# Kernel optimization log

Hardware: AMD Instinct MI355X
Metric: run time of the kernel (lower is better)

The kernel has to match this reference:

```python
import jax, jax.numpy as jnp
import numpy as np

B, T, DIM, H = 4, 2048, 1024, 16
HD = DIM // H  # 64
ROPE_BASE = 10000.0


def _rope_cos_sin(seq_len, head_dim, dtype):
    # lucidrains rotary-embedding-torch convention: interleaved pairs.
    inv_freq = 1.0 / (ROPE_BASE ** (jnp.arange(0, head_dim, 2, dtype=jnp.float32) / head_dim))
    freqs = jnp.arange(seq_len, dtype=jnp.float32)[:, None] * inv_freq[None, :]  # [T, hd/2]
    freqs = jnp.repeat(freqs, 2, axis=-1)  # [T, hd], each freq duplicated for the pair
    return jnp.cos(freqs).astype(dtype), jnp.sin(freqs).astype(dtype)


def _rotate_half(x):
    # interleaved pairs: (x1, x2) -> (-x2, x1)
    x = x.reshape(*x.shape[:-1], -1, 2)
    x1, x2 = x[..., 0], x[..., 1]
    return jnp.stack([-x2, x1], axis=-1).reshape(*x.shape[:-2], -1)


def _apply_rope(x, cos, sin):
    # x: [B, H, T, hd]; cos/sin: [T, hd]
    return x * cos[None, None, :, :] + _rotate_half(x) * sin[None, None, :, :]


def setup_inputs() -> dict:
    key = jax.random.key(0)
    kx, kqkv, kw, kb = jax.random.split(key, 4)
    s_qkv = 1.0 / np.sqrt(DIM)
    return {
        "x": jax.random.normal(kx, (B, T, DIM), dtype=jnp.float32),
        "w_qkv": jax.random.normal(kqkv, (3 * DIM, DIM), dtype=jnp.float32) * s_qkv,
        "w_proj": jax.random.normal(kw, (DIM, DIM), dtype=jnp.float32) * s_qkv,
        "b_proj": jax.random.normal(kb, (DIM,), dtype=jnp.float32) * 0.01,
    }


def reference(x, w_qkv, w_proj, b_proj):
    b, t, c = x.shape
    qkv = jnp.einsum('btc,dc->btd', x, w_qkv)  # [B, T, 3*C]
    qkv = qkv.reshape(b, t, 3, H, HD).transpose(2, 0, 3, 1, 4)  # [3, B, H, T, hd]
    q, k, v = qkv[0], qkv[1], qkv[2]

    cos, sin = _rope_cos_sin(t, HD, x.dtype)
    q = _apply_rope(q, cos, sin)
    k = _apply_rope(k, cos, sin)

    scale = 1.0 / np.sqrt(HD)
    scores = jnp.einsum('bhqd,bhkd->bhqk', q, k) * scale  # [B, H, T, T]
    attn = jax.nn.softmax(scores, axis=-1)
    out = jnp.einsum('bhqk,bhkd->bhqd', attn, v)  # [B, H, T, hd]

    out = out.transpose(0, 2, 1, 3).reshape(b, t, c)  # [B, T, C]
    return jnp.einsum('btc,dc->btd', out, w_proj) + b_proj
```

## Files before the change

kernel.cpp:

```cpp
#include <hip/hip_runtime.h>
#include <hip/hip_bf16.h>
#include <math.h>

#define Bz   4
#define Tz   2048
#define DIMz 1024
#define Hz   16
#define HDz  64
#define BHz  (Bz*Hz)
#define Mz   (Bz*Tz)
#define LOG2E 1.44269504088896340736f
#define QSCALE (0.125f * LOG2E)

typedef __attribute__((ext_vector_type(8)))  __bf16 bf16x8;
typedef __attribute__((ext_vector_type(4)))  __bf16 bf16x4;
typedef __attribute__((ext_vector_type(2)))  __bf16 bf16x2;
typedef __attribute__((ext_vector_type(4)))  float  f32x4;
typedef __attribute__((ext_vector_type(16))) float  f32x16;

__device__ __forceinline__ f32x4 mfma_16x16x32(bf16x8 a, bf16x8 b, f32x4 c) {
  return __builtin_amdgcn_mfma_f32_16x16x32_bf16(a, b, c, 0, 0, 0);
}
__device__ __forceinline__ f32x16 mfma_32x32x16(bf16x8 a, bf16x8 b, f32x16 c) {
  return __builtin_amdgcn_mfma_f32_32x32x16_bf16(a, b, c, 0, 0, 0);
}

__device__ __forceinline__ ushort f2bf(float f) {
  unsigned u = __float_as_uint(f);
  u += 0x7fffu + ((u >> 16) & 1u);
  return (ushort)(u >> 16);
}

__device__ __forceinline__ float fast_exp2(float x) {
#if __has_builtin(__builtin_amdgcn_exp2f)
  return __builtin_amdgcn_exp2f(x);
#else
  float r;
  asm("v_exp_f32 %0, %1\n\ts_nop 1" : "=v"(r) : "v"(x));
  return r;
#endif
}

__device__ __forceinline__ void gl_lds16(const ushort* g, ushort* l) {
  __builtin_amdgcn_global_load_lds(
      (const __attribute__((address_space(1))) unsigned int*)g,
      (__attribute__((address_space(3))) unsigned int*)l, 16, 0, 0);
}

#define N4_X   (Mz * DIMz / 4)
#define N4_WQ  (3 * DIMz * DIMz / 4)
#define N4_WP  (DIMz * DIMz / 4)
__global__ void k_cvt3(const float4* __restrict__ x,  ushort4* __restrict__ ox,
                       const float4* __restrict__ wq, ushort4* __restrict__ owq,
                       const float4* __restrict__ wp, ushort4* __restrict__ owp) {
  int i = blockIdx.x * blockDim.x + threadIdx.x;
  const float4* in; ushort4* out;
  if (i < N4_X)                { in = x + i;                 out = ox + i; }
  else if (i < N4_X + N4_WQ)   { in = wq + (i - N4_X);       out = owq + (i - N4_X); }
  else if (i < N4_X + N4_WQ + N4_WP) { in = wp + (i - N4_X - N4_WQ); out = owp + (i - N4_X - N4_WQ); }
  else return;
  float4 v = *in;
  ushort4 o;
  o.x = f2bf(v.x); o.y = f2bf(v.y); o.z = f2bf(v.z); o.w = f2bf(v.w);
  *out = o;
}

__global__ void k_rope_tab(float* __restrict__ tab) {
  int idx = blockIdx.x * blockDim.x + threadIdx.x;
  if (idx >= Tz * 32) return;
  int t = idx >> 5, i = idx & 31;
  double ang = (double)t * exp(((double)(-2 * i) / (double)HDz) * log(10000.0));
  tab[2 * idx]     = (float)cos(ang);
  tab[2 * idx + 1] = (float)sin(ang);
}


__global__ __launch_bounds__(256) void k_gemm_qkv(const ushort* __restrict__ A,
                                                  const ushort* __restrict__ Bw,
                                                  const float* __restrict__ tab,
                                                  ushort* __restrict__ qb,
                                                  ushort* __restrict__ kb,
                                                  ushort* __restrict__ vbt) {
  __shared__ ushort As[128 * 64];
  __shared__ ushort Bs[128 * 64];
  const int tid = threadIdx.x;
  const int xcd = blockIdx.x & 7;
  const int ib  = blockIdx.x >> 3;
  const int bm  = (xcd * 8 + (ib & 7)) << 7;
  const int bn  = (ib >> 3) << 7;
  const int wid = tid >> 6, lane = tid & 63;
  const int wr = (wid & 1) << 6, wc = (wid >> 1) << 6;
  const int lr = lane & 15, lg = lane >> 4;

  const int r8 = lane >> 3;
  const int cswz = (((lane & 7) ^ r8) << 3);
  const ushort* pA = A  + (size_t)(bm + wid * 8 + r8) * 1024 + cswz;
  const ushort* pB = Bw + (size_t)(bn + wid * 8 + r8) * 1024 + cswz;
  ushort* lA = &As[wid * 512];
  ushort* lB = &Bs[wid * 512];

  const int cs0 = ((lg ^ (lr & 7)) << 3);
  const int cs1 = cs0 ^ 32;

  const f32x4 fz = {0.f, 0.f, 0.f, 0.f};
  f32x4 acc[4][4];
  #pragma unroll
  for (int i = 0; i < 4; i++)
    #pragma unroll
    for (int j = 0; j < 4; j++) acc[i][j] = fz;

  for (int k0 = 0; k0 < 1024; k0 += 64) {
    __syncthreads();
    #pragma unroll
    for (int rep = 0; rep < 4; rep++) {
      gl_lds16(pA + (size_t)rep * 32768 + k0, lA + rep * 2048);
      gl_lds16(pB + (size_t)rep * 32768 + k0, lB + rep * 2048);
    }
    __syncthreads();
    #pragma unroll
    for (int kc = 0; kc < 2; kc++) {
      const int cs = kc ? cs1 : cs0;
      bf16x8 af[4], bfr[4];
      #pragma unroll
      for (int i = 0; i < 4; i++)
        af[i] = *reinterpret_cast<const bf16x8*>(&As[(wr + i * 16 + lr) * 64 + cs]);
      #pragma unroll
      for (int j = 0; j < 4; j++)
        bfr[j] = *reinterpret_cast<const bf16x8*>(&Bs[(wc + j * 16 + lr) * 64 + cs]);
      #pragma unroll
      for (int i = 0; i < 4; i++)
        #pragma unroll
        for (int j = 0; j < 4; j++)
          acc[i][j] = mfma_16x16x32(af[i], bfr[j], acc[i][j]);
    }
  }

  #pragma unroll
  for (int j = 0; j < 4; j++) {
    int col = bn + wc + j * 16 + lr;
    int which = col >> 10;
    int r = col & 1023;
    int h = r >> 6, hd = r & 63;
    #pragma unroll
    for (int i = 0; i < 4; i++) {
      int row0 = bm + wr + i * 16 + lg * 4;
      int b = row0 >> 11, t0 = row0 & 2047;
      if (which == 2) {
        int t0p = (t0 & ~12) | ((t0 & 4) << 1) | ((t0 & 8) >> 1);
        uint lo = (uint)f2bf(acc[i][j][0]) | ((uint)f2bf(acc[i][j][1]) << 16);
        uint hi = (uint)f2bf(acc[i][j][2]) | ((uint)f2bf(acc[i][j][3]) << 16);
        *reinterpret_cast<uint2*>(&vbt[((size_t)(b * Hz + h) * HDz + hd) * Tz + t0p]) =
            make_uint2(lo, hi);
      } else {
        ushort* dst = (which == 0) ? qb : kb;
        const float sc = (which == 0) ? QSCALE : 1.0f;
        const float sgn = (hd & 1) ? 1.0f : -1.0f;
        const float* tb = &tab[((size_t)t0 * 32 + (hd >> 1)) * 2];
        #pragma unroll
        for (int q = 0; q < 4; q++) {
          float own = acc[i][j][q];
          float other = __shfl_xor(own, 1);
          float c = tb[q * 64], s = tb[q * 64 + 1];
          dst[(((size_t)(b * Hz + h) * Tz + t0 + q) << 6) + hd] =
              f2bf((own * c + sgn * other * s) * sc);
        }
      }
    }
  }
}

__global__ __launch_bounds__(256, 4) void k_attn(const ushort* __restrict__ qb,
                                                 const ushort* __restrict__ kbp,
                                                 const ushort* __restrict__ vbt,
                                                 ushort* __restrict__ ao) {
  __shared__ ushort Ks0[64 * 64], Ks1[64 * 64], Ks2[64 * 64];
  __shared__ ushort Vs0[64 * 64], Vs1[64 * 64];

  const int bid = ((blockIdx.x & 7) << 7) + (blockIdx.x >> 3);
  const int qt = bid & 15;
  const int bh = bid >> 4;
  const int tid = threadIdx.x, wid = tid >> 6, lane = tid & 63;
  const int l31 = lane & 31, hi = lane >> 5;

  const ushort* Kg = kbp + (size_t)bh * Tz * HDz;
  const ushort* Vg = vbt + (size_t)bh * HDz * Tz;

  const ushort* Qrow = qb + ((size_t)bh * Tz + qt * 128 + wid * 32 + l31) * HDz + hi * 8;
  bf16x8 qf[4];
  #pragma unroll
  for (int m = 0; m < 4; m++)
    qf[m] = *reinterpret_cast<const bf16x8*>(Qrow + m * 16);

  const int r8 = lane >> 3;
  const int c0 = (((lane & 7) ^ r8 ^ ((2 * wid) & 3)) << 3);
  const int c1 = (((lane & 7) ^ r8 ^ ((2 * wid + 1) & 3)) << 3);
  const ushort* kp0 = Kg + (size_t)(wid * 16 + r8) * 64 + c0;
  const ushort* kp1 = Kg + (size_t)(wid * 16 + 8 + r8) * 64 + c1;
  const ushort* vp0 = Vg + (size_t)(wid * 16 + r8) * Tz + c0;
  const ushort* vp1 = Vg + (size_t)(wid * 16 + 8 + r8) * Tz + c1;

  f32x16 oacc0, oacc1;
  #pragma unroll
  for (int i = 0; i < 16; i++) { oacc0[i] = 0.f; oacc1[i] = 0.f; }
  float lrun = 0.f;

  const int swr = (lane & 7) ^ ((lane >> 3) & 3);
  int csk[4];
  #pragma unroll
  for (int m = 0; m < 4; m++) csk[m] = ((2 * m + hi) ^ swr) << 3;

  union FP { uint u[4]; bf16x8 v; };

  ushort *kb_cur = Ks0, *kb_nxt = Ks1, *kb_pre = Ks2;
  ushort *vb_cur = Vs0, *vb_nxt = Vs1;

  gl_lds16(kp0, kb_cur + wid * 1024); gl_lds16(kp1, kb_cur + wid * 1024 + 512);
  gl_lds16(kp0 + 4096, kb_nxt + wid * 1024); gl_lds16(kp1 + 4096, kb_nxt + wid * 1024 + 512);
  gl_lds16(vp0, vb_cur + wid * 1024); gl_lds16(vp1, vb_cur + wid * 1024 + 512);
  asm volatile("s_waitcnt vmcnt(4)" ::: "memory");
  __builtin_amdgcn_s_barrier();

  const int NT = Tz / 64;
  for (int kt = 0; kt < NT; kt++) {
    if (kt + 2 < NT) {
      gl_lds16(kp0 + (size_t)(kt + 2) * 4096, kb_pre + wid * 1024);
      gl_lds16(kp1 + (size_t)(kt + 2) * 4096, kb_pre + wid * 1024 + 512);
    }

    f32x16 sA, sB;
    #pragma unroll
    for (int i = 0; i < 16; i++) { sA[i] = 0.f; sB[i] = 0.f; }
    __builtin_amdgcn_s_setprio(1);
    #pragma unroll
    for (int m = 0; m < 4; m++) {
      bf16x8 kfA = *reinterpret_cast<const bf16x8*>(&kb_cur[l31 * 64 + csk[m]]);
      bf16x8 kfB = *reinterpret_cast<const bf16x8*>(&kb_cur[(32 + l31) * 64 + csk[m]]);
      sA = mfma_32x32x16(kfA, qf[m], sA);
      sB = mfma_32x32x16(kfB, qf[m], sB);
    }
    __builtin_amdgcn_s_setprio(0);

    float rs = 0.f;
    FP fA0, fA1, fB0, fB1;
    #pragma unroll
    for (int i = 0; i < 4; i++) {
      float e00 = fast_exp2(sA[2 * i]);
      float e01 = fast_exp2(sA[2 * i + 1]);
      float e10 = fast_exp2(sA[8 + 2 * i]);
      float e11 = fast_exp2(sA[9 + 2 * i]);
      rs += (e00 + e01) + (e10 + e11);
      bf16x2 t0, t1;
      t0[0] = (__bf16)e00; t0[1] = (__bf16)e01;
      t1[0] = (__bf16)e10; t1[1] = (__bf16)e11;
      fA0.u[i] = *reinterpret_cast<uint*>(&t0);
      fA1.u[i] = *reinterpret_cast<uint*>(&t1);
    }
    #pragma unroll
    for (int i = 0; i < 4; i++) {
      float e00 = fast_exp2(sB[2 * i]);
      float e01 = fast_exp2(sB[2 * i + 1]);
      float e10 = fast_exp2(sB[8 + 2 * i]);
      float e11 = fast_exp2(sB[9 + 2 * i]);
      rs += (e00 + e01) + (e10 + e11);
      bf16x2 t0, t1;
      t0[0] = (__bf16)e00; t0[1] = (__bf16)e01;
      t1[0] = (__bf16)e10; t1[1] = (__bf16)e11;
      fB0.u[i] = *reinterpret_cast<uint*>(&t0);
      fB1.u[i] = *reinterpret_cast<uint*>(&t1);
    }
    rs += __shfl_xor(rs, 32);
    lrun += rs;

    asm volatile("s_waitcnt vmcnt(2)" ::: "memory");
    __builtin_amdgcn_s_barrier();

    if (kt + 1 < NT) {
      gl_lds16(vp0 + (kt + 1) * 64, vb_nxt + wid * 1024);
      gl_lds16(vp1 + (kt + 1) * 64, vb_nxt + wid * 1024 + 512);
    }

    __builtin_amdgcn_s_setprio(1);
    #pragma unroll
    for (int blk = 0; blk < 2; blk++) {
      const ushort* vrow = &vb_cur[(blk * 32 + l31) * 64];
      bf16x8 vf0 = *reinterpret_cast<const bf16x8*>(vrow + csk[0]);
      bf16x8 vf1 = *reinterpret_cast<const bf16x8*>(vrow + csk[1]);
      bf16x8 vf2 = *reinterpret_cast<const bf16x8*>(vrow + csk[2]);
      bf16x8 vf3 = *reinterpret_cast<const bf16x8*>(vrow + csk[3]);
      f32x16 o = blk ? oacc1 : oacc0;
      o = mfma_32x32x16(fA0.v, vf0, o);
      o = mfma_32x32x16(fA1.v, vf1, o);
      o = mfma_32x32x16(fB0.v, vf2, o);
      o = mfma_32x32x16(fB1.v, vf3, o);
      if (blk) oacc1 = o; else oacc0 = o;
    }
    __builtin_amdgcn_s_setprio(0);

    ushort* t0 = kb_cur; kb_cur = kb_nxt; kb_nxt = kb_pre; kb_pre = t0;
    ushort* t1 = vb_cur; vb_cur = vb_nxt; vb_nxt = t1;
  }

  const int b = bh >> 4, h = bh & 15;
  #pragma unroll
  for (int r = 0; r < 16; r++) {
    int qrow = (r & 3) + 8 * (r >> 2) + 4 * hi;
    float inv = 1.0f / __shfl(lrun, qrow);
    int t = qt * 128 + wid * 32 + qrow;
    size_t base = ((size_t)(b * Tz + t) * Hz + h) * HDz;
    ao[base + l31]      = f2bf(oacc0[r] * inv);
    ao[base + 32 + l31] = f2bf(oacc1[r] * inv);
  }
}

__global__ __launch_bounds__(256) void k_gemm_proj(const ushort* __restrict__ A,
                                                   const ushort* __restrict__ Bw,
                                                   const float* __restrict__ bias,
                                                   float* __restrict__ out) {
  __shared__ ushort As[128 * 64];
  __shared__ ushort Bs[128 * 64];
  const int tid = threadIdx.x;
  const int xcd = blockIdx.x & 7;
  const int ib  = blockIdx.x >> 3;
  const int bm  = (xcd * 8 + (ib & 7)) << 7;
  const int bn  = (ib >> 3) << 7;
  const int wid = tid >> 6, lane = tid & 63;
  const int wr = (wid & 1) << 6, wc = (wid >> 1) << 6;
  const int lr = lane & 15, lg = lane >> 4;

  const int r8 = lane >> 3;
  const int cswz = (((lane & 7) ^ r8) << 3);
  const ushort* pA = A  + (size_t)(bm + wid * 8 + r8) * 1024 + cswz;
  const ushort* pB = Bw + (size_t)(bn + wid * 8 + r8) * 1024 + cswz;
  ushort* lA = &As[wid * 512];
  ushort* lB = &Bs[wid * 512];

  const int cs0 = ((lg ^ (lr & 7)) << 3);
  const int cs1 = cs0 ^ 32;

  const f32x4 fz = {0.f, 0.f, 0.f, 0.f};
  f32x4 acc[4][4];
  #pragma unroll
  for (int i = 0; i < 4; i++)
    #pragma unroll
    for (int j = 0; j < 4; j++) acc[i][j] = fz;

  for (int k0 = 0; k0 < 1024; k0 += 64) {
    __syncthreads();
    #pragma unroll
    for (int rep = 0; rep < 4; rep++) {
      gl_lds16(pA + (size_t)rep * 32768 + k0, lA + rep * 2048);
      gl_lds16(pB + (size_t)rep * 32768 + k0, lB + rep * 2048);
    }
    __syncthreads();
    #pragma unroll
    for (int kc = 0; kc < 2; kc++) {
      const int cs = kc ? cs1 : cs0;
      bf16x8 af[4], bfr[4];
      #pragma unroll
      for (int i = 0; i < 4; i++)
        af[i] = *reinterpret_cast<const bf16x8*>(&As[(wr + i * 16 + lr) * 64 + cs]);
      #pragma unroll
      for (int j = 0; j < 4; j++)
        bfr[j] = *reinterpret_cast<const bf16x8*>(&Bs[(wc + j * 16 + lr) * 64 + cs]);
      #pragma unroll
      for (int i = 0; i < 4; i++)
        #pragma unroll
        for (int j = 0; j < 4; j++)
          acc[i][j] = mfma_16x16x32(af[i], bfr[j], acc[i][j]);
    }
  }

  #pragma unroll
  for (int j = 0; j < 4; j++) {
    int col = bn + wc + j * 16 + lr;
    float bv = bias[col];
    #pragma unroll
    for (int i = 0; i < 4; i++) {
      #pragma unroll
      for (int q = 0; q < 4; q++) {
        int row = bm + wr + i * 16 + lg * 4 + q;
        out[(size_t)row * 1024 + col] = acc[i][j][q] + bv;
      }
    }
  }
}

extern "C" void kernel_launch(void* const* d_in, const int* in_sizes, int n_in,
                              void* d_out, int out_size, void* d_ws, size_t ws_size,
                              hipStream_t stream) {
  const float* x      = (const float*)d_in[0];
  const float* w_qkv  = (const float*)d_in[1];
  const float* w_proj = (const float*)d_in[2];
  const float* b_proj = (const float*)d_in[3];
  float* out = (float*)d_out;

  char* ws = (char*)d_ws;
  ushort* xh     = (ushort*)ws; ws += (size_t)Mz * DIMz * 2;
  ushort* wqkvh  = (ushort*)ws; ws += (size_t)3 * DIMz * DIMz * 2;
  ushort* wprojh = (ushort*)ws; ws += (size_t)DIMz * DIMz * 2;
  ushort* qbuf   = (ushort*)ws; ws += (size_t)BHz * Tz * HDz * 2;
  ushort* kbuf   = (ushort*)ws; ws += (size_t)BHz * Tz * HDz * 2;
  ushort* vbuft  = (ushort*)ws; ws += (size_t)BHz * HDz * Tz * 2;
  ushort* aout   = (ushort*)ws; ws += (size_t)Mz * DIMz * 2;
  float*  tab    = (float*)ws;  ws += (size_t)Tz * 32 * 2 * 4;

  k_cvt3<<<(N4_X + N4_WQ + N4_WP + 255) / 256, 256, 0, stream>>>(
      (const float4*)x, (ushort4*)xh,
      (const float4*)w_qkv, (ushort4*)wqkvh,
      (const float4*)w_proj, (ushort4*)wprojh);
  k_rope_tab<<<256, 256, 0, stream>>>(tab);
  k_gemm_qkv<<<64 * 24, 256, 0, stream>>>(xh, wqkvh, tab, qbuf, kbuf, vbuft);
  k_attn<<<BHz * (Tz / 128), 256, 0, stream>>>(qbuf, kbuf, vbuft, aout);
  k_gemm_proj<<<64 * 8, 256, 0, stream>>>(aout, wprojh, b_proj, out);
}
```

Before: 186.9 us.

## Triple-buffer GEMM LDS tiles with async prefetch and MFMA priority

Replaces the synchronous load-then-compute K loop in both the QKV and projection GEMMs with a three-stage LDS ring of 32-wide K tiles. Global-to-LDS loads for tile k+2 are issued before computing tile k, and partial vmcnt waits plus raw barriers replace the full syncthreads pairs. The MFMA block is wrapped in s_setprio to favour matrix issue. The aim is to hide global load latency behind compute, at the cost of more barriers (one per 32-wide K step), a new swizzle scheme, and hand-counted waitcnt values that must match the number of outstanding loads.

```diff
diff --git a/kernel.cpp b/kernel.cpp
--- a/kernel.cpp
+++ b/kernel.cpp
@@ -75,14 +75,73 @@
 }
 
 
+#define GEMM_PRE(Aptr, Bptr, bmv, bnv)                                              \
+  const int q4 = lane >> 2;                                                         \
+  const int cSW = (((lane & 3) ^ ((lane >> 3) & 3)) << 3);                          \
+  const ushort* sA = (Aptr) + (size_t)((bmv) + wid * 32 + q4) * 1024 + cSW;         \
+  const ushort* sB = (Bptr) + (size_t)((bnv) + wid * 32 + q4) * 1024 + cSW;         \
+  const int csf = ((lg ^ ((lr >> 1) & 3)) << 3);                                    \
+  ushort *aCur = SA0, *aNxt = SA1, *aPre = SA2;                                     \
+  ushort *bCur = SB0, *bNxt = SB1, *bPre = SB2;
+
+#define GEMM_STAGE(t, aDst, bDst)                                                   \
+  do {                                                                              \
+    gl_lds16(sA + (t) * 32, (aDst) + wid * 1024);                                   \
+    gl_lds16(sA + (t) * 32 + 16 * 1024, (aDst) + wid * 1024 + 512);                 \
+    gl_lds16(sB + (t) * 32, (bDst) + wid * 1024);                                   \
+    gl_lds16(sB + (t) * 32 + 16 * 1024, (bDst) + wid * 1024 + 512);                 \
+  } while (0)
+
+#define GEMM_COMPUTE()                                                              \
+  do {                                                                              \
+    bf16x8 af[4], bfr[4];                                                           \
+    _Pragma("unroll")                                                               \
+    for (int i = 0; i < 4; i++)                                                     \
+      af[i] = *reinterpret_cast<const bf16x8*>(&aCur[(wr + i * 16 + lr) * 32 + csf]); \
+    _Pragma("unroll")                                                               \
+    for (int j = 0; j < 4; j++)                                                     \
+      bfr[j] = *reinterpret_cast<const bf16x8*>(&bCur[(wc + j * 16 + lr) * 32 + csf]); \
+    __builtin_amdgcn_s_setprio(1);                                                  \
+    _Pragma("unroll")                                                               \
+    for (int i = 0; i < 4; i++)                                                     \
+      _Pragma("unroll")                                                             \
+      for (int j = 0; j < 4; j++)                                                   \
+        acc[i][j] = mfma_16x16x32(af[i], bfr[j], acc[i][j]);                        \
+    __builtin_amdgcn_s_setprio(0);                                                  \
+  } while (0)
+
+#define GEMM_ROTATE()                                                               \
+  do {                                                                              \
+    ushort* t0_ = aCur; aCur = aNxt; aNxt = aPre; aPre = t0_;                       \
+    ushort* t1_ = bCur; bCur = bNxt; bNxt = bPre; bPre = t1_;                       \
+  } while (0)
+
+#define GEMM_MAIN()                                                                 \
+  GEMM_STAGE(0, aCur, bCur);                                                        \
+  GEMM_STAGE(1, aNxt, bNxt);                                                        \
+  asm volatile("s_waitcnt vmcnt(4)" ::: "memory");                                  \
+  __builtin_amdgcn_s_barrier();                                                     \
+  for (int kt = 0; kt < 30; kt++) {                                                 \
+    GEMM_STAGE(kt + 2, aPre, bPre);                                                 \
+    GEMM_COMPUTE();                                                                 \
+    asm volatile("s_waitcnt vmcnt(4)" ::: "memory");                                \
+    __builtin_amdgcn_s_barrier();                                                   \
+    GEMM_ROTATE();                                                                  \
+  }                                                                                 \
+  GEMM_COMPUTE();                                                                   \
+  asm volatile("s_waitcnt vmcnt(0)" ::: "memory");                                  \
+  __builtin_amdgcn_s_barrier();                                                     \
+  GEMM_ROTATE();                                                                    \
+  GEMM_COMPUTE();
+
 __global__ __launch_bounds__(256) void k_gemm_qkv(const ushort* __restrict__ A,
                                                   const ushort* __restrict__ Bw,
                                                   const float* __restrict__ tab,
                                                   ushort* __restrict__ qb,
                                                   ushort* __restrict__ kb,
                                                   ushort* __restrict__ vbt) {
-  __shared__ ushort As[128 * 64];
-  __shared__ ushort Bs[128 * 64];
+  __shared__ ushort SA0[128 * 32], SA1[128 * 32], SA2[128 * 32];
+  __shared__ ushort SB0[128 * 32], SB1[128 * 32], SB2[128 * 32];
   const int tid = threadIdx.x;
   const int xcd = blockIdx.x & 7;
   const int ib  = blockIdx.x >> 3;
@@ -92,16 +151,6 @@
   const int wr = (wid & 1) << 6, wc = (wid >> 1) << 6;
   const int lr = lane & 15, lg = lane >> 4;
 
-  const int r8 = lane >> 3;
-  const int cswz = (((lane & 7) ^ r8) << 3);
-  const ushort* pA = A  + (size_t)(bm + wid * 8 + r8) * 1024 + cswz;
-  const ushort* pB = Bw + (size_t)(bn + wid * 8 + r8) * 1024 + cswz;
-  ushort* lA = &As[wid * 512];
-  ushort* lB = &Bs[wid * 512];
-
-  const int cs0 = ((lg ^ (lr & 7)) << 3);
-  const int cs1 = cs0 ^ 32;
-
   const f32x4 fz = {0.f, 0.f, 0.f, 0.f};
   f32x4 acc[4][4];
   #pragma unroll
@@ -109,31 +158,8 @@
     #pragma unroll
     for (int j = 0; j < 4; j++) acc[i][j] = fz;
 
-  for (int k0 = 0; k0 < 1024; k0 += 64) {
-    __syncthreads();
-    #pragma unroll
-    for (int rep = 0; rep < 4; rep++) {
-      gl_lds16(pA + (size_t)rep * 32768 + k0, lA + rep * 2048);
-      gl_lds16(pB + (size_t)rep * 32768 + k0, lB + rep * 2048);
-    }
-    __syncthreads();
-    #pragma unroll
-    for (int kc = 0; kc < 2; kc++) {
-      const int cs = kc ? cs1 : cs0;
-      bf16x8 af[4], bfr[4];
-      #pragma unroll
-      for (int i = 0; i < 4; i++)
-        af[i] = *reinterpret_cast<const bf16x8*>(&As[(wr + i * 16 + lr) * 64 + cs]);
-      #pragma unroll
-      for (int j = 0; j < 4; j++)
-        bfr[j] = *reinterpret_cast<const bf16x8*>(&Bs[(wc + j * 16 + lr) * 64 + cs]);
-      #pragma unroll
-      for (int i = 0; i < 4; i++)
-        #pragma unroll
-        for (int j = 0; j < 4; j++)
-          acc[i][j] = mfma_16x16x32(af[i], bfr[j], acc[i][j]);
-    }
-  }
+  GEMM_PRE(A, Bw, bm, bn);
+  GEMM_MAIN();
 
   #pragma unroll
   for (int j = 0; j < 4; j++) {
@@ -316,8 +342,8 @@
                                                    const ushort* __restrict__ Bw,
                                                    const float* __restrict__ bias,
                                                    float* __restrict__ out) {
-  __shared__ ushort As[128 * 64];
-  __shared__ ushort Bs[128 * 64];
+  __shared__ ushort SA0[128 * 32], SA1[128 * 32], SA2[128 * 32];
+  __shared__ ushort SB0[128 * 32], SB1[128 * 32], SB2[128 * 32];
   const int tid = threadIdx.x;
   const int xcd = blockIdx.x & 7;
   const int ib  = blockIdx.x >> 3;
@@ -327,16 +353,6 @@
   const int wr = (wid & 1) << 6, wc = (wid >> 1) << 6;
   const int lr = lane & 15, lg = lane >> 4;
 
-  const int r8 = lane >> 3;
-  const int cswz = (((lane & 7) ^ r8) << 3);
-  const ushort* pA = A  + (size_t)(bm + wid * 8 + r8) * 1024 + cswz;
-  const ushort* pB = Bw + (size_t)(bn + wid * 8 + r8) * 1024 + cswz;
-  ushort* lA = &As[wid * 512];
-  ushort* lB = &Bs[wid * 512];
-
-  const int cs0 = ((lg ^ (lr & 7)) << 3);
-  const int cs1 = cs0 ^ 32;
-
   const f32x4 fz = {0.f, 0.f, 0.f, 0.f};
   f32x4 acc[4][4];
   #pragma unroll
@@ -344,31 +360,8 @@
     #pragma unroll
     for (int j = 0; j < 4; j++) acc[i][j] = fz;
 
-  for (int k0 = 0; k0 < 1024; k0 += 64) {
-    __syncthreads();
-    #pragma unroll
-    for (int rep = 0; rep < 4; rep++) {
-      gl_lds16(pA + (size_t)rep * 32768 + k0, lA + rep * 2048);
-      gl_lds16(pB + (size_t)rep * 32768 + k0, lB + rep * 2048);
-    }
-    __syncthreads();
-    #pragma unroll
-    for (int kc = 0; kc < 2; kc++) {
-      const int cs = kc ? cs1 : cs0;
-      bf16x8 af[4], bfr[4];
-      #pragma unroll
-      for (int i = 0; i < 4; i++)
-        af[i] = *reinterpret_cast<const bf16x8*>(&As[(wr + i * 16 + lr) * 64 + cs]);
-      #pragma unroll
-      for (int j = 0; j < 4; j++)
-        bfr[j] = *reinterpret_cast<const bf16x8*>(&Bs[(wc + j * 16 + lr) * 64 + cs]);
-      #pragma unroll
-      for (int i = 0; i < 4; i++)
-        #pragma unroll
-        for (int j = 0; j < 4; j++)
-          acc[i][j] = mfma_16x16x32(af[i], bfr[j], acc[i][j]);
-    }
-  }
+  GEMM_PRE(A, Bw, bm, bn);
+  GEMM_MAIN();
 
   #pragma unroll
   for (int j = 0; j < 4; j++) {
```

Result: no change. 189.2 us (+1.2%).
